# Optimization experiments

Hardware: AMD Instinct MI355X
Metric: run time of the kernel (lower is better)

The kernel has to match this reference:

```python
import jax, jax.numpy as jnp
import numpy as np

C = 16                 # channels
N = 1048576            # number of latent vectors (points)
FILTERS = (1, 3, 3, 3, 1)
INIT_SCALE = 8.0
LIKELIHOOD_BOUND = 1e-9


def setup_inputs() -> dict:
    key = jax.random.key(0)
    ks = jax.random.split(key, 10)
    d = {
        "inputs": jax.random.normal(ks[0], (N, C), jnp.float32),
        "noise": jax.random.uniform(ks[1], (N, C), jnp.float32),  # shifted by -0.5 in reference
    }
    scale = INIT_SCALE ** (1.0 / 4.0)  # len(filters)+1 = 4 layers
    for i in range(4):
        fi, fo = FILTERS[i], FILTERS[i + 1]
        init_m = np.log(np.expm1(1.0 / scale / fo)).astype(np.float32)
        d[f"m{i}"] = jnp.full((C, fo, fi), init_m, dtype=jnp.float32)
        d[f"b{i}"] = jax.random.uniform(ks[2 + i], (C, fo, 1), jnp.float32, -0.5, 0.5)
        d[f"f{i}"] = jax.random.uniform(ks[6 + i], (C, fo, 1), jnp.float32, -0.1, 0.1)
    return d


def _logits_cumulative(x, ms, bs, fs):
    # x: [C, 1, N]; each layer: [C, fo, fi] @ [C, fi, N] -> [C, fo, N]
    logits = x
    for M, b, f in zip(ms, bs, fs):
        logits = jnp.einsum('cof,cfn->con', jax.nn.softplus(M), logits) + b
        logits = logits + jnp.tanh(f) * jnp.tanh(logits)
    return logits


def reference(inputs, noise, m0, b0, f0, m1, b1, f1, m2, b2, f2, m3, b3, f3):
    # quantize_mode='noise': additive uniform(-0.5, 0.5) noise
    outputs = inputs + (noise - 0.5)                 # [N, C]
    x = outputs.T[:, None, :]                        # [C, 1, N]
    ms = [m0, m1, m2, m3]; bs = [b0, b1, b2, b3]; fs = [f0, f1, f2, f3]
    lower = _logits_cumulative(x - 0.5, ms, bs, fs)  # [C, 1, N]
    upper = _logits_cumulative(x + 0.5, ms, bs, fs)  # [C, 1, N]
    sign = jax.lax.stop_gradient(-jnp.sign(lower + upper))
    likelihood = jnp.abs(jax.nn.sigmoid(sign * upper) - jax.nn.sigmoid(sign * lower))
    likelihood = likelihood.reshape(C, N).T          # [N, C]
    likelihood = jnp.maximum(likelihood, LIKELIHOOD_BOUND)  # Low_bound (fwd)
    return (outputs, likelihood)
```

## Files before the change

### kernel.cpp

```cpp
#include <hip/hip_runtime.h>
#include <math.h>

#define CH 16
#define NINT 256
#define NPTS (NINT + 1)
#define TAB_ELEMS (CH * NPTS)
#define ORIGIN 8.0f
#define INV_H 16.0f
#define ITERS 8


__device__ __forceinline__ float softplus_ref(float x) { return log1pf(expf(x)); }

__device__ float eval_net_exact(float x,
                                const float* sp0, const float* bb0, const float* tt0,
                                const float* sp1, const float* bb1, const float* tt1,
                                const float* sp2, const float* bb2, const float* tt2,
                                const float* sp3, float bb3, float tt3)
{
    float v0, v1, v2;
    {
        float l0 = fmaf(sp0[0], x, bb0[0]); v0 = fmaf(tt0[0], tanhf(l0), l0);
        float l1 = fmaf(sp0[1], x, bb0[1]); v1 = fmaf(tt0[1], tanhf(l1), l1);
        float l2 = fmaf(sp0[2], x, bb0[2]); v2 = fmaf(tt0[2], tanhf(l2), l2);
    }
    float w0, w1, w2;
    {
        float l0 = fmaf(sp1[0], v0, fmaf(sp1[1], v1, fmaf(sp1[2], v2, bb1[0])));
        float l1 = fmaf(sp1[3], v0, fmaf(sp1[4], v1, fmaf(sp1[5], v2, bb1[1])));
        float l2 = fmaf(sp1[6], v0, fmaf(sp1[7], v1, fmaf(sp1[8], v2, bb1[2])));
        w0 = fmaf(tt1[0], tanhf(l0), l0);
        w1 = fmaf(tt1[1], tanhf(l1), l1);
        w2 = fmaf(tt1[2], tanhf(l2), l2);
    }
    {
        float l0 = fmaf(sp2[0], w0, fmaf(sp2[1], w1, fmaf(sp2[2], w2, bb2[0])));
        float l1 = fmaf(sp2[3], w0, fmaf(sp2[4], w1, fmaf(sp2[5], w2, bb2[1])));
        float l2 = fmaf(sp2[6], w0, fmaf(sp2[7], w1, fmaf(sp2[8], w2, bb2[2])));
        v0 = fmaf(tt2[0], tanhf(l0), l0);
        v1 = fmaf(tt2[1], tanhf(l1), l1);
        v2 = fmaf(tt2[2], tanhf(l2), l2);
    }
    float l = fmaf(sp3[0], v0, fmaf(sp3[1], v1, fmaf(sp3[2], v2, bb3)));
    return fmaf(tt3, tanhf(l), l);
}

__global__ __launch_bounds__(256) void eb_table_kernel(
    const float* __restrict__ m0, const float* __restrict__ b0, const float* __restrict__ f0,
    const float* __restrict__ m1, const float* __restrict__ b1, const float* __restrict__ f1,
    const float* __restrict__ m2, const float* __restrict__ b2, const float* __restrict__ f2,
    const float* __restrict__ m3, const float* __restrict__ b3, const float* __restrict__ f3,
    float* __restrict__ tab)
{
    int t = blockIdx.x * blockDim.x + threadIdx.x;
    if (t >= TAB_ELEMS) return;
    int c = t / NPTS;
    int k = t - c * NPTS;

    float sp0[3], bb0[3], tt0[3];
    float sp1[9], bb1[3], tt1[3];
    float sp2[9], bb2[3], tt2[3];
    float sp3[3];
#pragma unroll
    for (int j = 0; j < 3; j++) {
        sp0[j] = softplus_ref(m0[c * 3 + j]);
        bb0[j] = b0[c * 3 + j];
        tt0[j] = tanhf(f0[c * 3 + j]);
        bb1[j] = b1[c * 3 + j];
        tt1[j] = tanhf(f1[c * 3 + j]);
        bb2[j] = b2[c * 3 + j];
        tt2[j] = tanhf(f2[c * 3 + j]);
        sp3[j] = softplus_ref(m3[c * 3 + j]);
    }
#pragma unroll
    for (int j = 0; j < 9; j++) {
        sp1[j] = softplus_ref(m1[c * 9 + j]);
        sp2[j] = softplus_ref(m2[c * 9 + j]);
    }
    float bb3 = b3[c];
    float tt3 = tanhf(f3[c]);

    float o = -ORIGIN + (float)k * (1.0f / INV_H);
    float lo = eval_net_exact(o - 0.5f, sp0, bb0, tt0, sp1, bb1, tt1, sp2, bb2, tt2, sp3, bb3, tt3);
    float up = eval_net_exact(o + 0.5f, sp0, bb0, tt0, sp1, bb1, tt1, sp2, bb2, tt2, sp3, bb3, tt3);

    float sum = lo + up;
    float s = (sum > 0.0f) ? -1.0f : ((sum < 0.0f) ? 1.0f : 0.0f);
    float su = 1.0f / (1.0f + expf(-s * up));
    float sl = 1.0f / (1.0f + expf(-s * lo));
    tab[t] = fmaxf(fabsf(su - sl), 1e-9f);
}


__device__ __forceinline__ float lookup(const float* lds, int row_base, float oe) {
    float t = fminf(fmaxf(fmaf(oe, INV_H, ORIGIN * INV_H), 0.0f), 255.999f);
    int i = (int)t;
    float fr = t - (float)i;
    const float* p = &lds[row_base + i];
    float v0 = p[0], v1 = p[1];
    return fmaxf(fmaf(fr, v1 - v0, v0), 1e-9f);
}

__global__ __launch_bounds__(256) void eb_main_kernel(
    const float4* __restrict__ inp, const float4* __restrict__ nz,
    const float* __restrict__ tab, float4* __restrict__ out, int nvec)
{
    __shared__ float lds[TAB_ELEMS];
    for (int j = threadIdx.x; j < TAB_ELEMS; j += 256) lds[j] = tab[j];

    const int tid = threadIdx.x;
    const int blockStart = blockIdx.x * (256 * ITERS);
    const int c0 = (tid & 3) * 4;
    const int r0 = (c0 + 0) * NPTS;
    const int r1 = (c0 + 1) * NPTS;
    const int r2 = (c0 + 2) * NPTS;
    const int r3 = (c0 + 3) * NPTS;

    float4 a[ITERS], b[ITERS];
#pragma unroll
    for (int k = 0; k < ITERS; k++) {
        int v = blockStart + k * 256 + tid;
        if (v < nvec) { a[k] = inp[v]; b[k] = nz[v]; }
    }

    __syncthreads();

#pragma unroll
    for (int k = 0; k < ITERS; k++) {
        int v = blockStart + k * 256 + tid;
        if (v >= nvec) break;
        float4 o, lik;
        o.x = a[k].x + b[k].x - 0.5f;
        o.y = a[k].y + b[k].y - 0.5f;
        o.z = a[k].z + b[k].z - 0.5f;
        o.w = a[k].w + b[k].w - 0.5f;
        lik.x = lookup(lds, r0, o.x);
        lik.y = lookup(lds, r1, o.y);
        lik.z = lookup(lds, r2, o.z);
        lik.w = lookup(lds, r3, o.w);
        out[v] = o;
        out[nvec + v] = lik;
    }
}


extern "C" void kernel_launch(void* const* d_in, const int* in_sizes, int n_in,
                              void* d_out, int out_size, void* d_ws, size_t ws_size,
                              hipStream_t stream) {
    const float* inp = (const float*)d_in[0];
    const float* nz  = (const float*)d_in[1];
    const float* m0 = (const float*)d_in[2];
    const float* b0 = (const float*)d_in[3];
    const float* f0 = (const float*)d_in[4];
    const float* m1 = (const float*)d_in[5];
    const float* b1 = (const float*)d_in[6];
    const float* f1 = (const float*)d_in[7];
    const float* m2 = (const float*)d_in[8];
    const float* b2 = (const float*)d_in[9];
    const float* f2 = (const float*)d_in[10];
    const float* m3 = (const float*)d_in[11];
    const float* b3 = (const float*)d_in[12];
    const float* f3 = (const float*)d_in[13];

    float* tab = (float*)d_ws;
    const int total = in_sizes[0];
    const int nvec = total >> 2;

    hipLaunchKernelGGL(eb_table_kernel, dim3((TAB_ELEMS + 255) / 256), dim3(256), 0, stream,
                       m0, b0, f0, m1, b1, f1, m2, b2, f2, m3, b3, f3, tab);

    const int chunk = 256 * ITERS;
    const int blocks = (nvec + chunk - 1) / chunk;
    hipLaunchKernelGGL(eb_main_kernel, dim3(blocks), dim3(256), 0, stream,
                       (const float4*)inp, (const float4*)nz, tab, (float4*)d_out, nvec);
}
```

Baseline: 272.3 us.

## Use grid-stride loop with nontemporal loads and stores in main kernel

Replaces the per-block batch of 8 prefetched float4 loads with a grid-stride loop over a fixed 2048-block grid. Global loads and stores now use nontemporal builtins on ext_vector float4 types. The aim is to amortize the per-block LDS table fill over more work and avoid polluting caches with streaming data. In exchange, each thread no longer batches independent loads, so fewer memory requests are in flight per thread.

```diff
diff --git a/kernel.cpp b/kernel.cpp
--- a/kernel.cpp
+++ b/kernel.cpp
@@ -7,7 +7,8 @@
 #define TAB_ELEMS (CH * NPTS)
 #define ORIGIN 8.0f
 #define INV_H 16.0f
-#define ITERS 8
+
+typedef float f32x4 __attribute__((ext_vector_type(4)));
 
 
 __device__ __forceinline__ float softplus_ref(float x) { return log1pf(expf(x)); }
@@ -102,44 +103,37 @@
 }
 
 __global__ __launch_bounds__(256) void eb_main_kernel(
-    const float4* __restrict__ inp, const float4* __restrict__ nz,
-    const float* __restrict__ tab, float4* __restrict__ out, int nvec)
+    const f32x4* __restrict__ inp, const f32x4* __restrict__ nz,
+    const float* __restrict__ tab, f32x4* __restrict__ out, int nvec)
 {
     __shared__ float lds[TAB_ELEMS];
     for (int j = threadIdx.x; j < TAB_ELEMS; j += 256) lds[j] = tab[j];
+    __syncthreads();
 
-    const int tid = threadIdx.x;
-    const int blockStart = blockIdx.x * (256 * ITERS);
-    const int c0 = (tid & 3) * 4;
+    const int gtid = blockIdx.x * 256 + threadIdx.x;
+    const int stride = gridDim.x * 256;
+    const int c0 = (gtid & 3) * 4;
     const int r0 = (c0 + 0) * NPTS;
     const int r1 = (c0 + 1) * NPTS;
     const int r2 = (c0 + 2) * NPTS;
     const int r3 = (c0 + 3) * NPTS;
 
-    float4 a[ITERS], b[ITERS];
-#pragma unroll
-    for (int k = 0; k < ITERS; k++) {
-        int v = blockStart + k * 256 + tid;
-        if (v < nvec) { a[k] = inp[v]; b[k] = nz[v]; }
-    }
+    for (int v = gtid; v < nvec; v += stride) {
+        f32x4 a = __builtin_nontemporal_load(&inp[v]);
+        f32x4 b = __builtin_nontemporal_load(&nz[v]);
 
-    __syncthreads();
-
-#pragma unroll
-    for (int k = 0; k < ITERS; k++) {
-        int v = blockStart + k * 256 + tid;
-        if (v >= nvec) break;
-        float4 o, lik;
-        o.x = a[k].x + b[k].x - 0.5f;
-        o.y = a[k].y + b[k].y - 0.5f;
-        o.z = a[k].z + b[k].z - 0.5f;
-        o.w = a[k].w + b[k].w - 0.5f;
+        f32x4 o, lik;
+        o.x = a.x + b.x - 0.5f;
+        o.y = a.y + b.y - 0.5f;
+        o.z = a.z + b.z - 0.5f;
+        o.w = a.w + b.w - 0.5f;
         lik.x = lookup(lds, r0, o.x);
         lik.y = lookup(lds, r1, o.y);
         lik.z = lookup(lds, r2, o.z);
         lik.w = lookup(lds, r3, o.w);
-        out[v] = o;
-        out[nvec + v] = lik;
+
+        __builtin_nontemporal_store(o, &out[v]);
+        __builtin_nontemporal_store(lik, &out[nvec + v]);
     }
 }
 
@@ -169,8 +163,6 @@
     hipLaunchKernelGGL(eb_table_kernel, dim3((TAB_ELEMS + 255) / 256), dim3(256), 0, stream,
                        m0, b0, f0, m1, b1, f1, m2, b2, f2, m3, b3, f3, tab);
 
-    const int chunk = 256 * ITERS;
-    const int blocks = (nvec + chunk - 1) / chunk;
-    hipLaunchKernelGGL(eb_main_kernel, dim3(blocks), dim3(256), 0, stream,
-                       (const float4*)inp, (const float4*)nz, tab, (float4*)d_out, nvec);
+    hipLaunchKernelGGL(eb_main_kernel, dim3(2048), dim3(256), 0, stream,
+                       (const f32x4*)inp, (const f32x4*)nz, tab, (f32x4*)d_out, nvec);
 }
```

Result: faster. 260.9 us (-4.2%).
